# Optimization experiments

Hardware: AMD Instinct MI355X
Metric: run time of the kernel (lower is better)

Reference implementation:

```python
import jax, jax.numpy as jnp
import numpy as np
from jax import lax

L = 5          # integration steps
B, H, W = 8, 256, 256
HID = 100      # res_block hidden channels
KS = 15        # gaussian kernel size
SIGMA = 4.0
MU = 0.02
SLOPE = 0.01   # LeakyReLU default slope


def setup_inputs() -> dict:
    key = jax.random.key(0)
    ks = jax.random.split(key, 7)
    source = jax.random.uniform(ks[0], (B, 1, H, W), jnp.float32)
    target = jax.random.uniform(ks[1], (B, 1, H, W), jnp.float32)
    source_seg = jax.random.uniform(ks[2], (B, 1, H, W), jnp.float32)
    z0 = jax.random.normal(ks[3], (1, 1, H, W), jnp.float32) * 0.01
    w1 = jax.random.normal(ks[4], (L, HID, 3, 3, 3), jnp.float32) / np.sqrt(3 * 9)
    w2 = jax.random.normal(ks[5], (L, HID, HID, 3, 3), jnp.float32) / np.sqrt(HID * 9)
    w3 = jax.random.normal(ks[6], (L, 1, HID, 3, 3), jnp.float32) / np.sqrt(HID * 9)
    return dict(source=source, target=target, source_seg=source_seg, z0=z0, w1=w1, w2=w2, w3=w3)


def _conv(x, w):
    return lax.conv_general_dilated(x, w, (1, 1), [(1, 1), (1, 1)],
                                    dimension_numbers=('NCHW', 'OIHW', 'NCHW'))


def _sobel(img):
    # kornia SpatialGradient(mode='sobel'), normalized kernel (/8), replicate padding
    kx = jnp.array([[-1., 0., 1.], [-2., 0., 2.], [-1., 0., 1.]], jnp.float32) / 8.0
    k = jnp.stack([kx, kx.T])[:, None]  # [2,1,3,3]: (dx, dy)
    xp = jnp.pad(img, ((0, 0), (0, 0), (1, 1), (1, 1)), mode='edge')
    return lax.conv_general_dilated(xp, k, (1, 1), 'VALID',
                                    dimension_numbers=('NCHW', 'OIHW', 'NCHW'))  # [B,2,H,W]


def _gauss1d():
    x = jnp.arange(KS, dtype=jnp.float32) - (KS - 1) / 2.0
    g = jnp.exp(-x * x / (2.0 * SIGMA * SIGMA))
    return g / g.sum()


def _gblur(x):
    # GaussianBlur2d, border_type='constant' (zero pad), separable
    b, c, h, w = x.shape
    g = _gauss1d()
    p = KS // 2
    xr = x.reshape(b * c, 1, h, w)
    xr = jnp.pad(xr, ((0, 0), (0, 0), (p, p), (0, 0)))
    xr = lax.conv_general_dilated(xr, g.reshape(1, 1, KS, 1), (1, 1), 'VALID',
                                  dimension_numbers=('NCHW', 'OIHW', 'NCHW'))
    xr = jnp.pad(xr, ((0, 0), (0, 0), (0, 0), (p, p)))
    xr = lax.conv_general_dilated(xr, g.reshape(1, 1, 1, KS), (1, 1), 'VALID',
                                  dimension_numbers=('NCHW', 'OIHW', 'NCHW'))
    return xr.reshape(b, c, h, w)


def _warp(img, grid):
    # bilinear grid_sample at absolute pixel coords, zeros outside (padding_mode='zeros')
    bc, c, hh, ww = img.shape
    x = grid[..., 0]
    y = grid[..., 1]
    x0 = jnp.floor(x)
    y0 = jnp.floor(y)
    x1 = x0 + 1.0
    y1 = y0 + 1.0

    def corner(xi, yi, wgt):
        inb = ((xi >= 0) & (xi <= ww - 1) & (yi >= 0) & (yi <= hh - 1)).astype(img.dtype)
        xc = jnp.clip(xi, 0, ww - 1).astype(jnp.int32)
        yc = jnp.clip(yi, 0, hh - 1).astype(jnp.int32)
        v = jax.vmap(lambda im, yy, xx: im[:, yy, xx])(img, yc, xc)  # [B,C,H,W]
        return v * (wgt * inb)[:, None, :, :]

    return (corner(x0, y0, (x1 - x) * (y1 - y)) + corner(x1, y0, (x - x0) * (y1 - y)) +
            corner(x0, y1, (x1 - x) * (y - y0)) + corner(x1, y1, (x - x0) * (y - y0)))


def _res_block(z, I, J, w1, w2, w3):
    # dropout is inference-mode identity
    x = jnp.concatenate([z, I, J], axis=1)
    x = jax.nn.leaky_relu(_conv(x, w1), SLOPE)
    x = jax.nn.leaky_relu(_conv(x, w2), SLOPE)
    return _conv(x, w3)


def _forward(source, target, z0, w1, w2, w3):
    bc = source.shape[0]
    gx, gy = jnp.meshgrid(jnp.arange(W, dtype=jnp.float32), jnp.arange(H, dtype=jnp.float32))
    id_grid = jnp.stack([gx, gy], axis=-1)[None]  # [1,H,W,2] pixel coords (x,y)

    image = source
    residuals = [jnp.broadcast_to(z0, (bc, 1, H, W)).astype(source.dtype)]
    fields, grads, phi_list = [], [], []
    for i in range(L):
        g = _sobel(image)                                  # [B,2,H,W]
        grads.append(g)
        field = _gblur(-residuals[i] * g).transpose(0, 2, 3, 1)  # [B,H,W,2]
        fields.append(field)
        deformation = id_grid - field / L                  # [B,H,W,2]
        f = _res_block(residuals[i], image, target, w1[i], w2[i], w3[i]) / L
        residuals.append(residuals[i] - f)
        if i != 0:
            phi_list = [_warp(p.transpose(0, 3, 1, 2), deformation).transpose(0, 2, 3, 1)
                        for p in phi_list]
        phi_list.append(deformation)
        rs = residuals[-1]
        for k in range(len(residuals) - 2):
            rs = rs + _warp(residuals[k + 1], phi_list[k + 1])
        image = _warp(source, phi_list[0]) + rs * (MU * MU) / L
    return image, jnp.stack(fields), jnp.stack(residuals), jnp.stack(grads)


def reference(source, target, source_seg, z0, w1, w2, w3):
    # source_seg is unused in the original forward
    return _forward(source, target, z0, w1, w2, w3)
```

## Files before the change

### kernel.cpp

```cpp
#include <hip/hip_runtime.h>
#include <math.h>

typedef __attribute__((ext_vector_type(8))) short short8;
typedef __attribute__((ext_vector_type(4))) float f32x4;
typedef unsigned int uint;
typedef unsigned short ushort;

#define Lsteps 5
#define Hn 256
#define Wn 256
#define HWn 65536
#define BHW 524288

#define OUT_IMG    0
#define OUT_FIELDS 524288
#define OUT_RES    5767168
#define OUT_GRADS  8912896

#define WS_IMG   0
#define WS_PHIA  524288
#define WS_PHIB  5767168
#define WS_VTMP  11010048
#define WS_W2B   12058624
#define WS_W3P   12381184
#define WS_X2    12386944

__device__ inline float lrelu(float s) { return s > 0.f ? s : 0.01f * s; }

__device__ inline ushort bf16r(float f) {
  uint u = __float_as_uint(f);
  return (ushort)((u + 0x7fffu + ((u >> 16) & 1u)) >> 16);
}

__device__ inline void make_gauss(float* G) {
  float s = 0.f;
#pragma unroll
  for (int t = 0; t < 15; t++) {
    float d = (float)t - 7.f;
    G[t] = expf(-d * d * (1.f / 32.f));
    s += G[t];
  }
  float inv = 1.f / s;
#pragma unroll
  for (int t = 0; t < 15; t++) G[t] *= inv;
}

__device__ inline float bilin1(const float* __restrict__ p, float x, float y) {
  float x0f = floorf(x), y0f = floorf(y);
  int x0 = (int)x0f, y0 = (int)y0f;
  float fx = x - x0f, fy = y - y0f;
  float w00 = (1.f - fx) * (1.f - fy), w10 = fx * (1.f - fy);
  float w01 = (1.f - fx) * fy, w11 = fx * fy;
  float acc = 0.f;
  if ((unsigned)x0 < 256u && (unsigned)y0 < 256u) acc += w00 * p[y0 * 256 + x0];
  if ((unsigned)(x0 + 1) < 256u && (unsigned)y0 < 256u) acc += w10 * p[y0 * 256 + x0 + 1];
  if ((unsigned)x0 < 256u && (unsigned)(y0 + 1) < 256u) acc += w01 * p[(y0 + 1) * 256 + x0];
  if ((unsigned)(x0 + 1) < 256u && (unsigned)(y0 + 1) < 256u) acc += w11 * p[(y0 + 1) * 256 + x0 + 1];
  return acc;
}

__device__ inline void bilin2(const float* __restrict__ p, float x, float y,
                              float& o0, float& o1) {
  float x0f = floorf(x), y0f = floorf(y);
  int x0 = (int)x0f, y0 = (int)y0f;
  float fx = x - x0f, fy = y - y0f;
  float w00 = (1.f - fx) * (1.f - fy), w10 = fx * (1.f - fy);
  float w01 = (1.f - fx) * fy, w11 = fx * fy;
  o0 = 0.f; o1 = 0.f;
  if ((unsigned)x0 < 256u && (unsigned)y0 < 256u) {
    const float* q = p + (y0 * 256 + x0) * 2; o0 += w00 * q[0]; o1 += w00 * q[1];
  }
  if ((unsigned)(x0 + 1) < 256u && (unsigned)y0 < 256u) {
    const float* q = p + (y0 * 256 + x0 + 1) * 2; o0 += w10 * q[0]; o1 += w10 * q[1];
  }
  if ((unsigned)x0 < 256u && (unsigned)(y0 + 1) < 256u) {
    const float* q = p + ((y0 + 1) * 256 + x0) * 2; o0 += w01 * q[0]; o1 += w01 * q[1];
  }
  if ((unsigned)(x0 + 1) < 256u && (unsigned)(y0 + 1) < 256u) {
    const float* q = p + ((y0 + 1) * 256 + x0 + 1) * 2; o0 += w11 * q[0]; o1 += w11 * q[1];
  }
}

__global__ void init_res0_kernel(const float* __restrict__ z0, float* __restrict__ res0) {
  int idx = blockIdx.x * 256 + threadIdx.x;
  res0[idx] = z0[idx & 65535];
}

__global__ void w2b_prep(const float* __restrict__ w2, ushort* __restrict__ w2b) {
  int idx = blockIdx.x * 256 + threadIdx.x;
  if (idx >= Lsteps * 129024) return;
  int l = idx / 129024;
  int r = idx - l * 129024;
  int tap = r / 14336;
  int r2 = r - tap * 14336;
  int kc = r2 / 3584;
  int r3 = r2 - kc * 3584;
  int o = r3 >> 9;
  int r4 = r3 & 511;
  int lane = r4 >> 3;
  int j = r4 & 7;
  int q = lane >> 4, n = lane & 15;
  int oc = o * 16 + n;
  int ic = kc * 32 + q * 8 + j;
  float v = (oc < 100 && ic < 100) ? w2[l * 90000 + oc * 900 + ic * 9 + tap] : 0.f;
  w2b[idx] = bf16r(v);
}

__global__ void w3p_prep(const float* __restrict__ w3, float* __restrict__ w3p) {
  int idx = blockIdx.x * 256 + threadIdx.x;
  if (idx >= Lsteps * 9 * 128) return;
  int l = idx / 1152;
  int r = idx - l * 1152;
  int tap = r >> 7;
  int ic = r & 127;
  w3p[idx] = (ic < 100) ? w3[l * 900 + ic * 9 + tap] : 0.f;
}

__global__ __launch_bounds__(256) void field_fused(
    const float* __restrict__ img, const float* __restrict__ res_i,
    float* __restrict__ grads_i, float* __restrict__ fields_i) {
  __shared__ float sBuf[2560];
  __shared__ float sP[2][2400];
  const int tid = threadIdx.x;
  const int b = blockIdx.z;
  const int Y0 = blockIdx.y * 16, X0 = blockIdx.x * 64;
  float G[15]; make_gauss(G);
  const float* ib = img + b * HWn;
  const float* rb = res_i + b * HWn;

  for (int u = tid; u < 2560; u += 256) {
    int ly = u / 80, lx = u - ly * 80;
    int gy = Y0 - 8 + ly, gx = X0 - 8 + lx;
    gy = gy < 0 ? 0 : (gy > 255 ? 255 : gy);
    gx = gx < 0 ? 0 : (gx > 255 ? 255 : gx);
    sBuf[u] = ib[gy * 256 + gx];
  }
  __syncthreads();

  for (int u = tid; u < 2400; u += 256) {
    int ly = u / 80, lx = u - ly * 80;
    int gy = Y0 - 7 + ly, gx = X0 - 7 + lx;
    float p0 = 0.f, p1 = 0.f;
    if (lx < 78 && (unsigned)gy < 256u && (unsigned)gx < 256u) {
      int base = (ly + 1) * 80 + (lx + 1);
      float a00 = sBuf[base - 81], a01 = sBuf[base - 80], a02 = sBuf[base - 79];
      float a10 = sBuf[base - 1], a12 = sBuf[base + 1];
      float a20 = sBuf[base + 79], a21 = sBuf[base + 80], a22 = sBuf[base + 81];
      float gxs = (a02 - a00 + 2.f * (a12 - a10) + a22 - a20) * 0.125f;
      float gys = (a20 - a00 + 2.f * (a21 - a01) + a22 - a02) * 0.125f;
      float r = rb[gy * 256 + gx];
      p0 = -r * gxs; p1 = -r * gys;
      if (ly >= 7 && ly < 23 && lx >= 7 && lx < 71) {
        grads_i[b * 131072 + gy * 256 + gx] = gxs;
        grads_i[b * 131072 + 65536 + gy * 256 + gx] = gys;
      }
    }
    sP[0][u] = p0; sP[1][u] = p1;
  }
  __syncthreads();

  for (int u = tid; u < 2560; u += 256) {
    int c = u >= 1280 ? 1 : 0;
    int v = u - c * 1280;
    int ly = v / 80, lx = v - ly * 80;
    float s = 0.f;
    if (lx < 78) {
      const float* pc = &sP[c][ly * 80 + lx];
#pragma unroll
      for (int t = 0; t < 15; t++) s += G[t] * pc[t * 80];
    }
    sBuf[u] = s;
  }
  __syncthreads();

  for (int u = tid; u < 2048; u += 256) {
    int c = u >> 10, v = u & 1023;
    int ly = v >> 6, lx = v & 63;
    const float* tc = sBuf + c * 1280 + ly * 80 + lx;
    float s = 0.f;
#pragma unroll
    for (int t = 0; t < 15; t++) s += G[t] * tc[t];
    int gy = Y0 + ly, gx = X0 + lx;
    fields_i[(b * 65536 + gy * 256 + gx) * 2 + c] = s;
  }
}

__global__ __launch_bounds__(256, 3) void conv12_kernel(
    const float* __restrict__ res_i, const float* __restrict__ img,
    const float* __restrict__ tgt, const float* __restrict__ w1,
    const short8* __restrict__ w2b, ushort* __restrict__ x2) {
  __shared__ ushort x1s[180 * 136];
  const int tid = threadIdx.x;
  const int b = blockIdx.z;
  const int Y0 = blockIdx.y * 8, X0 = blockIdx.x * 16;
  const float* zb = res_i + b * HWn;
  const float* ib = img + b * HWn;
  const float* tb = tgt + b * HWn;

  if (tid < 180) {
    int ly = tid / 18, lx = tid - ly * 18;
    int gy = Y0 + ly - 1, gx = X0 + lx - 1;
    const bool inb = (unsigned)gy < 256u && (unsigned)gx < 256u;
    float p[27];
#pragma unroll
    for (int dy = 0; dy < 3; dy++)
#pragma unroll
      for (int dx = 0; dx < 3; dx++) {
        int yy = gy + dy - 1, xx = gx + dx - 1;
        bool ok = (unsigned)yy < 256u && (unsigned)xx < 256u;
        int o = ok ? (yy * 256 + xx) : 0;
        int j = dy * 3 + dx;
        p[j] = ok ? zb[o] : 0.f;
        p[9 + j] = ok ? ib[o] : 0.f;
        p[18 + j] = ok ? tb[o] : 0.f;
      }
    const uint base = (uint)tid * 136u;
    for (int oc = 0; oc < 100; oc += 2) {
      const float* wa = w1 + oc * 27;
      float s0 = 0.f, s1 = 0.f;
#pragma unroll
      for (int j = 0; j < 27; j++) {
        s0 = fmaf(p[j], wa[j], s0);
        s1 = fmaf(p[j], wa[27 + j], s1);
      }
      s0 = inb ? lrelu(s0) : 0.f;
      s1 = inb ? lrelu(s1) : 0.f;
      *(uint*)&x1s[base + oc] = (uint)bf16r(s0) | ((uint)bf16r(s1) << 16);
    }
#pragma unroll
    for (int oc = 100; oc < 128; oc += 2) *(uint*)&x1s[base + oc] = 0u;
  }
  __syncthreads();

  const int lane = tid & 63, wv = tid >> 6;
  const int q = lane >> 4, n = lane & 15;
  f32x4 acc[2][7];
#pragma unroll
  for (int r = 0; r < 2; r++)
#pragma unroll
    for (int o = 0; o < 7; o++) acc[r][o] = (f32x4)(0.f);

  const short8* wsrc = w2b + lane;
  auto loadw = [&](short8 (&dst)[7], int it) {
    const short8* s = wsrc + (it >> 2) * 1792 + (it & 3) * 448;
#pragma unroll
    for (int o = 0; o < 7; o++) dst[o] = s[o * 64];
  };
  auto compute = [&](short8 (&w)[7], int it) {
    const int tap = it >> 2, kc = it & 3;
    const int dy = tap / 3, dx = tap - dy * 3;
    const uint arow0 = (uint)((wv * 2 + dy) * 18 + n + dx) * 136u + (uint)(kc * 32 + q * 8);
    short8 a0 = *(const short8*)&x1s[arow0];
    short8 a1 = *(const short8*)&x1s[arow0 + 2448u];
    __builtin_amdgcn_s_setprio(1);
#pragma unroll
    for (int o = 0; o < 7; o++) {
      acc[0][o] = __builtin_amdgcn_mfma_f32_16x16x32_bf16(a0, w[o], acc[0][o], 0, 0, 0);
      acc[1][o] = __builtin_amdgcn_mfma_f32_16x16x32_bf16(a1, w[o], acc[1][o], 0, 0, 0);
    }
    __builtin_amdgcn_s_setprio(0);
  };

  short8 wA[7], wB[7];
  loadw(wA, 0);
#pragma unroll
  for (int it = 0; it < 36; it += 2) {
    loadw(wB, it + 1);
    compute(wA, it);
    if (it + 2 < 36) loadw(wA, it + 2);
    compute(wB, it + 1);
  }

  __syncthreads();
#pragma unroll
  for (int r = 0; r < 2; r++) {
    const int py = (wv * 2 + r) * 16;
#pragma unroll
    for (int o = 0; o < 7; o++) {
      if (o == 6 && n >= 8) continue;
      const int oc = o * 16 + n;
#pragma unroll
      for (int v = 0; v < 4; v++) {
        const int pix = py + q * 4 + v;
        x1s[pix * 104 + oc] = bf16r(lrelu(acc[r][o][v]));
      }
    }
  }
  __syncthreads();
  ushort* xg = x2 + (size_t)((b << 16) + Y0 * 256 + X0) * 104;
  for (int u = tid; u < 1664; u += 256) {
    int pix = u / 13, ch = u - pix * 13;
    int y = pix >> 4, x = pix & 15;
    uint4 val = *(const uint4*)&x1s[pix * 104 + ch * 8];
    *(uint4*)(xg + (size_t)(y * 256 + x) * 104 + ch * 8) = val;
  }
}

__global__ __launch_bounds__(256, 2) void cpi_fused(
    const float* __restrict__ res_i,
    const ushort* __restrict__ x2,
    const float* __restrict__ w3p,
    const float* __restrict__ fields_i,
    const float* __restrict__ phi_src,
    float* __restrict__ phi_dst,
    const float* __restrict__ source,
    const float* __restrict__ res_base,
    float* __restrict__ res_n,
    float* __restrict__ img_out, int step) {
  __shared__ ushort sx[324 * 104];
  const int tid = threadIdx.x;
  const int b = blockIdx.z;
  const int Y0 = blockIdx.y * 16, X0 = blockIdx.x * 16;

  for (int u = tid; u < 4212; u += 256) {
    int pix = u / 13, ch = u - pix * 13;
    int py = pix / 18, px = pix - py * 18;
    int gy = Y0 - 1 + py, gx = X0 - 1 + px;
    uint4 v = make_uint4(0u, 0u, 0u, 0u);
    if ((unsigned)gy < 256u && (unsigned)gx < 256u)
      v = *(const uint4*)(x2 + (size_t)((b << 16) + gy * 256 + gx) * 104 + ch * 8);
    *(uint4*)&sx[pix * 104 + ch * 8] = v;
  }
  __syncthreads();

  const int ly = tid >> 4, lx = tid & 15;
  const int y = Y0 + ly, x = X0 + lx;
  const int idx = (b << 16) + y * 256 + x;

  float acc = 0.f;
#pragma unroll
  for (int tap = 0; tap < 9; tap++) {
    int dy = tap / 3, dx = tap - dy * 3;
    const ushort* px_ = &sx[((ly + dy) * 18 + (lx + dx)) * 104];
    const float* wt = w3p + tap * 128;
#pragma unroll
    for (int c = 0; c < 13; c++) {
      uint4 u = *(const uint4*)(px_ + c * 8);
      const float* w8 = wt + c * 8;
      acc = fmaf(__uint_as_float(u.x << 16), w8[0], acc);
      acc = fmaf(__uint_as_float(u.x & 0xffff0000u), w8[1], acc);
      acc = fmaf(__uint_as_float(u.y << 16), w8[2], acc);
      acc = fmaf(__uint_as_float(u.y & 0xffff0000u), w8[3], acc);
      acc = fmaf(__uint_as_float(u.z << 16), w8[4], acc);
      acc = fmaf(__uint_as_float(u.z & 0xffff0000u), w8[5], acc);
      acc = fmaf(__uint_as_float(u.w << 16), w8[6], acc);
      acc = fmaf(__uint_as_float(u.w & 0xffff0000u), w8[7], acc);
    }
  }
  float rn = res_i[idx] - 0.2f * acc;
  res_n[idx] = rn;

  int pix2 = (y * 256 + x) * 2;
  float f0 = fields_i[2 * idx], f1 = fields_i[2 * idx + 1];
  float dxp = (float)x - f0 * 0.2f;
  float dyp = (float)y - f1 * 0.2f;
  float img = 0.f, rs = rn;
  for (int k = 0; k <= step; k++) {
    float o0, o1;
    if (k == step) { o0 = dxp; o1 = dyp; }
    else bilin2(phi_src + (size_t)(k * 8 + b) * 131072, dxp, dyp, o0, o1);
    float* dst = phi_dst + (size_t)(k * 8 + b) * 131072 + pix2;
    dst[0] = o0; dst[1] = o1;
    if (k == 0) img = bilin1(source + b * HWn, o0, o1);
    else rs += bilin1(res_base + (size_t)k * BHW + b * HWn, o0, o1);
  }
  img_out[idx] = img + rs * 8.0e-5f;
}

extern "C" void kernel_launch(void* const* d_in, const int* in_sizes, int n_in,
                              void* d_out, int out_size, void* d_ws, size_t ws_size,
                              hipStream_t stream) {
  const float* source = (const float*)d_in[0];
  const float* target = (const float*)d_in[1];
  const float* z0 = (const float*)d_in[3];
  const float* w1 = (const float*)d_in[4];
  const float* w2 = (const float*)d_in[5];
  const float* w3 = (const float*)d_in[6];
  float* out = (float*)d_out;
  float* ws = (float*)d_ws;

  float* ws_img = ws + WS_IMG;
  float* phiA = ws + WS_PHIA;
  float* phiB = ws + WS_PHIB;
  ushort* w2b = (ushort*)(ws + WS_W2B);
  float* w3p = ws + WS_W3P;
  ushort* x2 = (ushort*)(ws + WS_X2);

  hipMemcpyAsync(ws_img, source, BHW * sizeof(float), hipMemcpyDeviceToDevice, stream);
  init_res0_kernel<<<BHW / 256, 256, 0, stream>>>(z0, out + OUT_RES);
  w2b_prep<<<(Lsteps * 129024 + 255) / 256, 256, 0, stream>>>(w2, w2b);
  w3p_prep<<<23, 256, 0, stream>>>(w3, w3p);

  for (int i = 0; i < Lsteps; i++) {
    float* grads_i = out + OUT_GRADS + (size_t)i * 1048576;
    float* fields_i = out + OUT_FIELDS + (size_t)i * 1048576;
    const float* res_i = out + OUT_RES + (size_t)i * BHW;
    float* res_n = out + OUT_RES + (size_t)(i + 1) * BHW;
    float* phi_dst = (i % 2 == 0) ? phiA : phiB;
    float* phi_src = (i % 2 == 0) ? phiB : phiA;

    field_fused<<<dim3(4, 16, 8), 256, 0, stream>>>(ws_img, res_i, grads_i, fields_i);
    conv12_kernel<<<dim3(16, 32, 8), 256, 0, stream>>>(
        res_i, ws_img, target, w1 + i * 2700,
        (const short8*)(w2b + (size_t)i * 129024), x2);
    cpi_fused<<<dim3(16, 16, 8), 256, 0, stream>>>(
        res_i, x2, w3p + i * 1152, fields_i, phi_src, phi_dst,
        source, out + OUT_RES, res_n, ws_img, i);
  }
  hipMemcpyAsync(out + OUT_IMG, ws_img, BHW * sizeof(float), hipMemcpyDeviceToDevice, stream);
}
```

Baseline: 1.489 ms.

## Repartition conv2 MFMA work: waves split output channels instead of pixel rows

Each wave in the hidden-layer conv now covers all 8 pixel rows of the tile for 2 output-channel blocks, instead of 2 rows for all 7 channel blocks. Per wave this cuts global weight fragment loads from 7 to 2 per iteration, at the cost of 8 LDS activation reads instead of 2. The goal is to reduce global/L2 weight traffic and register pressure from the weight double buffer. The fourth wave computes an extra padded block (o=7), which adds redundant MFMA work that is thrown away. Its weight reads for that block run past the end of the channel data, but the results are masked at writeback.

```diff
diff --git a/kernel.cpp b/kernel.cpp
--- a/kernel.cpp
+++ b/kernel.cpp
@@ -234,34 +234,33 @@
 
   const int lane = tid & 63, wv = tid >> 6;
   const int q = lane >> 4, n = lane & 15;
-  f32x4 acc[2][7];
-#pragma unroll
-  for (int r = 0; r < 2; r++)
-#pragma unroll
-    for (int o = 0; o < 7; o++) acc[r][o] = (f32x4)(0.f);
-
-  const short8* wsrc = w2b + lane;
-  auto loadw = [&](short8 (&dst)[7], int it) {
+  f32x4 acc[8][2];
+#pragma unroll
+  for (int r = 0; r < 8; r++)
+#pragma unroll
+    for (int f = 0; f < 2; f++) acc[r][f] = (f32x4)(0.f);
+
+  const short8* wsrc = w2b + lane + (uint)(wv * 2) * 64u;
+  auto loadw = [&](short8 (&dst)[2], int it) {
     const short8* s = wsrc + (it >> 2) * 1792 + (it & 3) * 448;
-#pragma unroll
-    for (int o = 0; o < 7; o++) dst[o] = s[o * 64];
+    dst[0] = s[0];
+    dst[1] = s[64];
   };
-  auto compute = [&](short8 (&w)[7], int it) {
+  auto compute = [&](short8 (&w)[2], int it) {
     const int tap = it >> 2, kc = it & 3;
     const int dy = tap / 3, dx = tap - dy * 3;
-    const uint arow0 = (uint)((wv * 2 + dy) * 18 + n + dx) * 136u + (uint)(kc * 32 + q * 8);
-    short8 a0 = *(const short8*)&x1s[arow0];
-    short8 a1 = *(const short8*)&x1s[arow0 + 2448u];
+    const uint abase = (uint)(dy * 18 + n + dx) * 136u + (uint)(kc * 32 + q * 8);
     __builtin_amdgcn_s_setprio(1);
 #pragma unroll
-    for (int o = 0; o < 7; o++) {
-      acc[0][o] = __builtin_amdgcn_mfma_f32_16x16x32_bf16(a0, w[o], acc[0][o], 0, 0, 0);
-      acc[1][o] = __builtin_amdgcn_mfma_f32_16x16x32_bf16(a1, w[o], acc[1][o], 0, 0, 0);
+    for (int r = 0; r < 8; r++) {
+      short8 a = *(const short8*)&x1s[abase + (uint)r * 2448u];
+      acc[r][0] = __builtin_amdgcn_mfma_f32_16x16x32_bf16(a, w[0], acc[r][0], 0, 0, 0);
+      acc[r][1] = __builtin_amdgcn_mfma_f32_16x16x32_bf16(a, w[1], acc[r][1], 0, 0, 0);
     }
     __builtin_amdgcn_s_setprio(0);
   };
 
-  short8 wA[7], wB[7];
+  short8 wA[2], wB[2];
   loadw(wA, 0);
 #pragma unroll
   for (int it = 0; it < 36; it += 2) {
@@ -273,16 +272,19 @@
 
   __syncthreads();
 #pragma unroll
-  for (int r = 0; r < 2; r++) {
-    const int py = (wv * 2 + r) * 16;
-#pragma unroll
-    for (int o = 0; o < 7; o++) {
-      if (o == 6 && n >= 8) continue;
+  for (int f = 0; f < 2; f++) {
+    const int o = wv * 2 + f;
+    if (o < 7) {
       const int oc = o * 16 + n;
-#pragma unroll
-      for (int v = 0; v < 4; v++) {
-        const int pix = py + q * 4 + v;
-        x1s[pix * 104 + oc] = bf16r(lrelu(acc[r][o][v]));
+      if (oc < 104) {
+#pragma unroll
+        for (int r = 0; r < 8; r++) {
+#pragma unroll
+          for (int v = 0; v < 4; v++) {
+            const int pix = r * 16 + q * 4 + v;
+            x1s[pix * 104 + oc] = bf16r(lrelu(acc[r][f][v]));
+          }
+        }
       }
     }
   }
```

Result: no change. 1.489 ms (-0.1%).
